# Kernel optimization log

Hardware: AMD Instinct MI355X
Metric: run time of the kernel (lower is better)

The kernel has to match this reference:

```python
import jax, jax.numpy as jnp
import numpy as np

NUM_FREQS = 10
N_POINTS = 500000
NUM_CLUSTERS = 64
KNN = 4
INPUT_CH = 3 + 3 * 2 * NUM_FREQS  # 63


def embed(x):
    # NeRF-style positional encoding: [x, sin(2^f x), cos(2^f x)] -> [N, 63]
    freqs = 2.0 ** jnp.arange(NUM_FREQS, dtype=x.dtype)          # [F]
    xf = x[:, None, :] * freqs[:, None]                           # [N, F, 3]
    n = x.shape[0]
    return jnp.concatenate(
        [x, jnp.sin(xf).reshape(n, -1), jnp.cos(xf).reshape(n, -1)], axis=-1)


def setup_inputs() -> dict:
    key = jax.random.key(0)
    ks = jax.random.split(key, 8)
    X = jax.random.normal(ks[0], (N_POINTS, 3), dtype=jnp.float32)
    cluster_ids = jax.random.randint(ks[1], (N_POINTS, KNN), 0, NUM_CLUSTERS)
    dist = jax.random.uniform(ks[2], (KNN, N_POINTS), dtype=jnp.float32)
    W_lin = jax.random.normal(ks[3], (NUM_CLUSTERS * 3, INPUT_CH), dtype=jnp.float32) * 0.05
    lambdas = jnp.ones((NUM_CLUSTERS,), dtype=jnp.float32) * 15.0
    # Only the first KNN MLPs can ever be dispatched (nearest = argmin over KNN rows)
    W0 = jax.random.normal(ks[4], (KNN, 256, 3 + INPUT_CH), dtype=jnp.float32) * 0.05
    W1 = jax.random.normal(ks[5], (KNN, 256, 256), dtype=jnp.float32) * 0.05
    W2 = jax.random.normal(ks[6], (KNN, 3, 256), dtype=jnp.float32) * 0.05
    return {"X": X, "cluster_ids": cluster_ids, "dist": dist, "W_lin": W_lin,
            "lambdas": lambdas, "W0": W0, "W1": W1, "W2": W2}


def _mlp(w0, w1, w2, x):
    h = jax.nn.relu(x @ w0.T)
    h = jax.nn.relu(h @ w1.T)
    return jnp.tanh(h @ w2.T)


def reference(X, cluster_ids, dist, W_lin, lambdas, W0, W1, W2):
    n = X.shape[0]
    # masked-out rays (-1,-1,-1) produce zeros; all math is per-point so we
    # compute densely and zero the masked rows at the end
    mask = (X[:, 0] == -1.0) & (X[:, 1] == -1.0) & (X[:, 2] == -1.0)  # [N]

    enc = embed(X)                                  # [N, 63]
    nearest = jnp.argmin(dist, axis=0)              # [N], values in [0, KNN)
    lam = lambdas[nearest]                          # [N]
    weights = jax.nn.softmax(lam * jnp.exp(-lam * dist), axis=0)  # [KNN, N]

    # per-cluster linear heads: [N, num_clusters, 3]
    lin = (enc @ W_lin.T).reshape(n, -1, 3)
    # knn gather + softmax-weighted combine -> [N, 3]
    gathered = jnp.take_along_axis(lin, cluster_ids[:, :, None], axis=1)  # [N, K, 3]
    combined = jnp.sum(gathered * weights.T[:, :, None], axis=1)          # [N, 3]

    inp = jnp.concatenate([combined, enc], axis=1)  # [N, 66]
    rgb = jnp.zeros((n, 3), dtype=X.dtype)
    for k in range(KNN):  # small fixed expert count
        out_k = _mlp(W0[k], W1[k], W2[k], inp)
        rgb = jnp.where((nearest == k)[:, None], out_k, rgb)

    return jnp.where(mask[:, None], 0.0, rgb)
```

## Files before the change

kernel.cpp:

```cpp
#include <hip/hip_runtime.h>
#include <cstdint>
#include <cstddef>

typedef _Float16 f16x8 __attribute__((ext_vector_type(8)));
typedef float    f32x4 __attribute__((ext_vector_type(4)));

#define TILE_M 128
#define WROWS  32

__global__ __launch_bounds__(256)
void k0_split(const float* __restrict__ W0, const float* __restrict__ W1,
              const float* __restrict__ W2, const float* __restrict__ Wlin,
              _Float16* __restrict__ W0h, _Float16* __restrict__ W0l,
              _Float16* __restrict__ W1h, _Float16* __restrict__ W1l,
              _Float16* __restrict__ W2h, _Float16* __restrict__ W2l,
              _Float16* __restrict__ WlinH, _Float16* __restrict__ WlinL)
{
    int idx = blockIdx.x * 256 + threadIdx.x;
    if (idx < 4*256*96) {
        int k = idx % 96; int en = idx / 96;
        float v = (k < 66) ? W0[en*66 + k] : 0.f;
        _Float16 h = (_Float16)v;
        W0h[idx] = h; W0l[idx] = (_Float16)(v - (float)h);
    }
    if (idx < 4*256*256) {
        float v = W1[idx];
        _Float16 h = (_Float16)v;
        W1h[idx] = h; W1l[idx] = (_Float16)(v - (float)h);
    }
    if (idx < 4*16*256) {
        int k = idx % 256; int er = idx / 256;
        int e = er / 16; int r = er % 16;
        float v = (r < 3) ? W2[(e*3 + r)*256 + k] : 0.f;
        _Float16 h = (_Float16)v;
        W2h[idx] = h; W2l[idx] = (_Float16)(v - (float)h);
    }
    if (idx < 192*64) {
        int k = idx & 63; int cc = idx >> 6;
        float v = (k < 63) ? Wlin[cc*63 + k] : 0.f;
        _Float16 h = (_Float16)v;
        WlinH[idx] = h; WlinL[idx] = (_Float16)(v - (float)h);
    }
}

#define MFMA16(A,B,C) __builtin_amdgcn_mfma_f32_16x16x32_f16(A, B, C, 0, 0, 0)

__global__ __launch_bounds__(256)
void k1_prep(const float* __restrict__ X, const int* __restrict__ cid,
             const float* __restrict__ dist,
             const _Float16* __restrict__ WlinH, const _Float16* __restrict__ WlinL,
             const float* __restrict__ lambdas,
             float* __restrict__ combined, int* __restrict__ order,
             int* __restrict__ cnt, int N)
{
    __shared__ _Float16 lins[4][32][200];
    __shared__ int hist[4];
    __shared__ int baseoff[4];
    int t = threadIdx.x;
    int wv = t >> 6, lane = t & 63, q = lane >> 4, lm = lane & 15;
    int blk = blockIdx.x;
    if (t < 4) hist[t] = 0;

    float xx[2][3];
    #pragma unroll
    for (int mt = 0; mt < 2; mt++) {
        int p = blk*128 + wv*32 + mt*16 + lm;
        bool v = (p < N);
        xx[mt][0] = v ? X[p*3+0] : 0.f;
        xx[mt][1] = v ? X[p*3+1] : 0.f;
        xx[mt][2] = v ? X[p*3+2] : 0.f;
    }
    f32x4 acc[2][12];
    #pragma unroll
    for (int mt = 0; mt < 2; mt++)
        #pragma unroll
        for (int nt = 0; nt < 12; nt++)
            acc[mt][nt] = (f32x4){0.f, 0.f, 0.f, 0.f};

    #pragma unroll
    for (int ks = 0; ks < 2; ks++) {
        f16x8 ah[2], al[2];
        #pragma unroll
        for (int mt = 0; mt < 2; mt++) {
            #pragma unroll
            for (int j = 0; j < 8; j++) {
                int c = ks*32 + q*8 + j;
                float v;
                if (c >= 63) v = 0.f;
                else if (c < 3) v = xx[mt][c];
                else {
                    int is_sin = (c < 33);
                    int s = is_sin ? (c - 3) : (c - 33);
                    int f = s / 3;
                    int d = s - f*3;
                    float arg = xx[mt][d] * (float)(1 << f);
                    float sv, cv;
                    sincosf(arg, &sv, &cv);
                    v = is_sin ? sv : cv;
                }
                _Float16 h = (_Float16)v;
                ah[mt][j] = h;
                al[mt][j] = (_Float16)(v - (float)h);
            }
        }
        #pragma unroll
        for (int nt = 0; nt < 12; nt++) {
            f16x8 bh = *(const f16x8*)(WlinH + (nt*16 + lm)*64 + ks*32 + q*8);
            f16x8 bl = *(const f16x8*)(WlinL + (nt*16 + lm)*64 + ks*32 + q*8);
            #pragma unroll
            for (int mt = 0; mt < 2; mt++) {
                acc[mt][nt] = MFMA16(ah[mt], bh, acc[mt][nt]);
                acc[mt][nt] = MFMA16(ah[mt], bl, acc[mt][nt]);
                acc[mt][nt] = MFMA16(al[mt], bh, acc[mt][nt]);
            }
        }
    }
    #pragma unroll
    for (int mt = 0; mt < 2; mt++)
        #pragma unroll
        for (int nt = 0; nt < 12; nt++)
            #pragma unroll
            for (int r = 0; r < 4; r++)
                lins[wv][mt*16 + q*4 + r][nt*16 + lm] = (_Float16)acc[mt][nt][r];
    __syncthreads();

    int near = 0, lrank = 0; bool valid = false; int p = 0;
    if (t < 128) {
        p = blk*128 + t;
        valid = (p < N);
        if (valid) {
            float d[4];
            #pragma unroll
            for (int k = 0; k < 4; k++) d[k] = dist[(size_t)k*N + p];
            float dmin = d[0]; near = 0;
            #pragma unroll
            for (int k = 1; k < 4; k++) if (d[k] < dmin) { dmin = d[k]; near = k; }
            float lam = lambdas[near];
            float s[4], wgt[4];
            #pragma unroll
            for (int k = 0; k < 4; k++) s[k] = lam * expf(-lam * d[k]);
            float m = fmaxf(fmaxf(s[0], s[1]), fmaxf(s[2], s[3]));
            float ssum = 0.f;
            #pragma unroll
            for (int k = 0; k < 4; k++) { wgt[k] = expf(s[k] - m); ssum += wgt[k]; }
            float inv = 1.f / ssum;
            int4 c4 = *(const int4*)(cid + p*4);
            int cks[4] = {c4.x, c4.y, c4.z, c4.w};
            int wv2 = t >> 5, r2 = t & 31;
            float c0 = 0.f, c1 = 0.f, c2 = 0.f;
            #pragma unroll
            for (int k = 0; k < 4; k++) {
                float wk = wgt[k] * inv;
                int b = cks[k] * 3;
                c0 += wk * (float)lins[wv2][r2][b+0];
                c1 += wk * (float)lins[wv2][r2][b+1];
                c2 += wk * (float)lins[wv2][r2][b+2];
            }
            combined[p*3+0] = c0; combined[p*3+1] = c1; combined[p*3+2] = c2;
            lrank = atomicAdd(&hist[near], 1);
        }
    }
    __syncthreads();
    if (t < 4) baseoff[t] = atomicAdd(&cnt[t], hist[t]);
    __syncthreads();
    if (valid) order[(size_t)near*N + baseoff[near] + lrank] = p;
}

__global__ __launch_bounds__(256, 1)
void k4_mlp(const float* __restrict__ X, const float* __restrict__ combined,
            const int* __restrict__ order, const int* __restrict__ cnt,
            const _Float16* __restrict__ W0h, const _Float16* __restrict__ W0l,
            const _Float16* __restrict__ W1h, const _Float16* __restrict__ W1l,
            const _Float16* __restrict__ W2h, const _Float16* __restrict__ W2l,
            float* __restrict__ out, int N, int tpe)
{
    __shared__ __align__(16) float hbuf[4][32][268];
    int e = blockIdx.x & 3;
    int tile = blockIdx.x >> 2;
    int count = cnt[e];
    int row0 = tile * TILE_M;
    if (row0 >= count) return;
    int wv   = threadIdx.x >> 6;
    int lane = threadIdx.x & 63;
    int q    = lane >> 4;
    int lm   = lane & 15;
    int wbase = row0 + wv * WROWS;
    const int* ord = order + (size_t)e * N + wbase;

    float xx[2][3], cb[2][3];
    #pragma unroll
    for (int mt = 0; mt < 2; mt++) {
        int r = mt*16 + lm;
        int pos = wbase + r;
        int p = (pos < count) ? ord[r] : 0;
        xx[mt][0] = X[p*3+0]; xx[mt][1] = X[p*3+1]; xx[mt][2] = X[p*3+2];
        cb[mt][0] = combined[p*3+0]; cb[mt][1] = combined[p*3+1]; cb[mt][2] = combined[p*3+2];
    }

    const _Float16* w0hb = W0h + e*(256*96);
    const _Float16* w0lb = W0l + e*(256*96);
    f32x4 acc[2][16];
    #pragma unroll
    for (int mt = 0; mt < 2; mt++)
        #pragma unroll
        for (int nt = 0; nt < 16; nt++)
            acc[mt][nt] = (f32x4){0.f, 0.f, 0.f, 0.f};

    #pragma unroll
    for (int ks = 0; ks < 3; ks++) {
        f16x8 ah[2], al[2];
        #pragma unroll
        for (int mt = 0; mt < 2; mt++) {
            #pragma unroll
            for (int j = 0; j < 8; j++) {
                int c = ks*32 + q*8 + j;
                float v;
                if (c >= 66) v = 0.f;
                else if (c < 3) v = (c==0) ? cb[mt][0] : ((c==1) ? cb[mt][1] : cb[mt][2]);
                else if (c < 6) v = (c==3) ? xx[mt][0] : ((c==4) ? xx[mt][1] : xx[mt][2]);
                else {
                    int is_sin = (c < 36);
                    int s = is_sin ? (c - 6) : (c - 36);
                    int f = s / 3;
                    int d = s - f*3;
                    float xd = (d==0) ? xx[mt][0] : ((d==1) ? xx[mt][1] : xx[mt][2]);
                    float arg = xd * (float)(1 << f);
                    float sv, cv;
                    sincosf(arg, &sv, &cv);
                    v = is_sin ? sv : cv;
                }
                _Float16 h = (_Float16)v;
                ah[mt][j] = h;
                al[mt][j] = (_Float16)(v - (float)h);
            }
        }
        #pragma unroll
        for (int nt = 0; nt < 16; nt++) {
            f16x8 bh = *(const f16x8*)(w0hb + (nt*16 + lm)*96 + ks*32 + q*8);
            f16x8 bl = *(const f16x8*)(w0lb + (nt*16 + lm)*96 + ks*32 + q*8);
            #pragma unroll
            for (int mt = 0; mt < 2; mt++) {
                acc[mt][nt] = MFMA16(ah[mt], bh, acc[mt][nt]);
                acc[mt][nt] = MFMA16(ah[mt], bl, acc[mt][nt]);
                acc[mt][nt] = MFMA16(al[mt], bh, acc[mt][nt]);
            }
        }
    }
    #pragma unroll
    for (int mt = 0; mt < 2; mt++)
        #pragma unroll
        for (int nt = 0; nt < 16; nt++)
            #pragma unroll
            for (int r = 0; r < 4; r++)
                hbuf[wv][mt*16 + q*4 + r][nt*16 + lm] = fmaxf(acc[mt][nt][r], 0.f);
    __syncthreads();

    const _Float16* w1hb = W1h + e*(256*256);
    const _Float16* w1lb = W1l + e*(256*256);
    #pragma unroll
    for (int mt = 0; mt < 2; mt++)
        #pragma unroll
        for (int nt = 0; nt < 16; nt++)
            acc[mt][nt] = (f32x4){0.f, 0.f, 0.f, 0.f};
    for (int ks = 0; ks < 8; ks++) {
        f16x8 ah[2], al[2];
        #pragma unroll
        for (int mt = 0; mt < 2; mt++) {
            const float* src = &hbuf[wv][mt*16 + lm][ks*32 + q*8];
            f32x4 va0 = *(const f32x4*)(src);
            f32x4 va1 = *(const f32x4*)(src + 4);
            #pragma unroll
            for (int j = 0; j < 8; j++) {
                float v = (j < 4) ? va0[j] : va1[j-4];
                _Float16 h = (_Float16)v;
                ah[mt][j] = h;
                al[mt][j] = (_Float16)(v - (float)h);
            }
        }
        #pragma unroll
        for (int nt = 0; nt < 16; nt++) {
            f16x8 bh = *(const f16x8*)(w1hb + (nt*16 + lm)*256 + ks*32 + q*8);
            f16x8 bl = *(const f16x8*)(w1lb + (nt*16 + lm)*256 + ks*32 + q*8);
            #pragma unroll
            for (int mt = 0; mt < 2; mt++) {
                acc[mt][nt] = MFMA16(ah[mt], bh, acc[mt][nt]);
                acc[mt][nt] = MFMA16(ah[mt], bl, acc[mt][nt]);
                acc[mt][nt] = MFMA16(al[mt], bh, acc[mt][nt]);
            }
        }
    }
    __syncthreads();
    #pragma unroll
    for (int mt = 0; mt < 2; mt++)
        #pragma unroll
        for (int nt = 0; nt < 16; nt++)
            #pragma unroll
            for (int r = 0; r < 4; r++)
                hbuf[wv][mt*16 + q*4 + r][nt*16 + lm] = fmaxf(acc[mt][nt][r], 0.f);
    __syncthreads();

    const _Float16* w2hb = W2h + e*(16*256);
    const _Float16* w2lb = W2l + e*(16*256);
    f32x4 acc3[2];
    acc3[0] = (f32x4){0.f,0.f,0.f,0.f};
    acc3[1] = (f32x4){0.f,0.f,0.f,0.f};
    for (int ks = 0; ks < 8; ks++) {
        f16x8 ah[2], al[2];
        #pragma unroll
        for (int mt = 0; mt < 2; mt++) {
            const float* src = &hbuf[wv][mt*16 + lm][ks*32 + q*8];
            f32x4 va0 = *(const f32x4*)(src);
            f32x4 va1 = *(const f32x4*)(src + 4);
            #pragma unroll
            for (int j = 0; j < 8; j++) {
                float v = (j < 4) ? va0[j] : va1[j-4];
                _Float16 h = (_Float16)v;
                ah[mt][j] = h;
                al[mt][j] = (_Float16)(v - (float)h);
            }
        }
        f16x8 bh = *(const f16x8*)(w2hb + lm*256 + ks*32 + q*8);
        f16x8 bl = *(const f16x8*)(w2lb + lm*256 + ks*32 + q*8);
        #pragma unroll
        for (int mt = 0; mt < 2; mt++) {
            acc3[mt] = MFMA16(ah[mt], bh, acc3[mt]);
            acc3[mt] = MFMA16(ah[mt], bl, acc3[mt]);
            acc3[mt] = MFMA16(al[mt], bh, acc3[mt]);
        }
    }
    if (lm < 3) {
        #pragma unroll
        for (int mt = 0; mt < 2; mt++)
            #pragma unroll
            for (int r = 0; r < 4; r++) {
                int row = mt*16 + q*4 + r;
                int pos = wbase + row;
                if (pos < count) {
                    int p = ord[row];
                    float x0 = X[p*3+0], x1 = X[p*3+1], x2 = X[p*3+2];
                    float msk = (x0 == -1.f && x1 == -1.f && x2 == -1.f) ? 0.f : 1.f;
                    out[p*3 + lm] = tanhf(acc3[mt][r]) * msk;
                }
            }
    }
}

extern "C" void kernel_launch(void* const* d_in, const int* in_sizes, int n_in,
                              void* d_out, int out_size, void* d_ws, size_t ws_size,
                              hipStream_t stream)
{
    const float* X    = (const float*)d_in[0];
    const int*   cid  = (const int*)  d_in[1];
    const float* dist = (const float*)d_in[2];
    const float* Wlin = (const float*)d_in[3];
    const float* lam  = (const float*)d_in[4];
    const float* W0   = (const float*)d_in[5];
    const float* W1   = (const float*)d_in[6];
    const float* W2   = (const float*)d_in[7];
    float* out = (float*)d_out;
    int N = in_sizes[0] / 3;

    char* ws = (char*)d_ws;
    size_t off = 0;
    int* cnt = (int*)(ws + off);           off += 256;
    float* combined = (float*)(ws + off);  off += (size_t)N * 3 * sizeof(float);
    off = (off + 255) & ~(size_t)255;
    int* order = (int*)(ws + off);         off += (size_t)4 * N * sizeof(int);
    off = (off + 255) & ~(size_t)255;
    _Float16* W0h = (_Float16*)(ws + off); off += (size_t)4*256*96*2;
    _Float16* W0l = (_Float16*)(ws + off); off += (size_t)4*256*96*2;
    _Float16* W1h = (_Float16*)(ws + off); off += (size_t)4*256*256*2;
    _Float16* W1l = (_Float16*)(ws + off); off += (size_t)4*256*256*2;
    _Float16* W2h = (_Float16*)(ws + off); off += (size_t)4*16*256*2;
    _Float16* W2l = (_Float16*)(ws + off); off += (size_t)4*16*256*2;
    _Float16* WlinH = (_Float16*)(ws + off); off += (size_t)192*64*2;
    _Float16* WlinL = (_Float16*)(ws + off); off += (size_t)192*64*2;

    hipMemsetAsync(cnt, 0, 4 * sizeof(int), stream);
    k0_split<<<dim3((4*256*256 + 255)/256), dim3(256), 0, stream>>>(
        W0, W1, W2, Wlin, W0h, W0l, W1h, W1l, W2h, W2l, WlinH, WlinL);
    k1_prep<<<dim3((N + 127)/128), dim3(256), 0, stream>>>(
        X, cid, dist, WlinH, WlinL, lam, combined, order, cnt, N);
    int tpe = (N + TILE_M - 1) / TILE_M;
    k4_mlp<<<dim3(4*tpe), dim3(256), 0, stream>>>(
        X, combined, order, cnt, W0h, W0l, W1h, W1l, W2h, W2l, out, N, tpe);
}
```

Before: 1.117 ms.

## Halve MLP tile rows per wave for two blocks per CU with setprio

Each wave of the expert-MLP kernel now handles 16 rows instead of 32, so the tile drops to 64 rows and the shared buffer shrinks to half. With the accumulator registers halved, launch bounds allow two blocks per CU, and the block-wide syncthreads are removed because each wave only touches its own shared slice. s_setprio is raised around the MFMA loops so waves that are issuing matrix work get scheduling priority. The cost is that each weight fragment loaded from memory now feeds half as many MFMAs, so weight traffic per point doubles.

```diff
diff --git a/kernel.cpp b/kernel.cpp
--- a/kernel.cpp
+++ b/kernel.cpp
@@ -5,8 +5,7 @@
 typedef _Float16 f16x8 __attribute__((ext_vector_type(8)));
 typedef float    f32x4 __attribute__((ext_vector_type(4)));
 
-#define TILE_M 128
-#define WROWS  32
+#define TILE_M 64
 
 __global__ __launch_bounds__(256)
 void k0_split(const float* __restrict__ W0, const float* __restrict__ W1,
@@ -166,7 +165,7 @@
     if (valid) order[(size_t)near*N + baseoff[near] + lrank] = p;
 }
 
-__global__ __launch_bounds__(256, 1)
+__global__ __launch_bounds__(256, 2)
 void k4_mlp(const float* __restrict__ X, const float* __restrict__ combined,
             const int* __restrict__ order, const int* __restrict__ cnt,
             const _Float16* __restrict__ W0h, const _Float16* __restrict__ W0l,
@@ -174,7 +173,7 @@
             const _Float16* __restrict__ W2h, const _Float16* __restrict__ W2l,
             float* __restrict__ out, int N, int tpe)
 {
-    __shared__ __align__(16) float hbuf[4][32][268];
+    __shared__ __align__(16) float hbuf[4][16][268];
     int e = blockIdx.x & 3;
     int tile = blockIdx.x >> 2;
     int count = cnt[e];
@@ -184,164 +183,137 @@
     int lane = threadIdx.x & 63;
     int q    = lane >> 4;
     int lm   = lane & 15;
-    int wbase = row0 + wv * WROWS;
+    int wbase = row0 + wv * 16;
     const int* ord = order + (size_t)e * N + wbase;
 
-    float xx[2][3], cb[2][3];
-    #pragma unroll
-    for (int mt = 0; mt < 2; mt++) {
-        int r = mt*16 + lm;
-        int pos = wbase + r;
-        int p = (pos < count) ? ord[r] : 0;
-        xx[mt][0] = X[p*3+0]; xx[mt][1] = X[p*3+1]; xx[mt][2] = X[p*3+2];
-        cb[mt][0] = combined[p*3+0]; cb[mt][1] = combined[p*3+1]; cb[mt][2] = combined[p*3+2];
+    float xx[3], cb[3];
+    {
+        int pos = wbase + lm;
+        int p = (pos < count) ? ord[lm] : 0;
+        xx[0] = X[p*3+0]; xx[1] = X[p*3+1]; xx[2] = X[p*3+2];
+        cb[0] = combined[p*3+0]; cb[1] = combined[p*3+1]; cb[2] = combined[p*3+2];
     }
 
     const _Float16* w0hb = W0h + e*(256*96);
     const _Float16* w0lb = W0l + e*(256*96);
-    f32x4 acc[2][16];
-    #pragma unroll
-    for (int mt = 0; mt < 2; mt++)
-        #pragma unroll
-        for (int nt = 0; nt < 16; nt++)
-            acc[mt][nt] = (f32x4){0.f, 0.f, 0.f, 0.f};
+    f32x4 acc[16];
+    #pragma unroll
+    for (int nt = 0; nt < 16; nt++)
+        acc[nt] = (f32x4){0.f, 0.f, 0.f, 0.f};
 
     #pragma unroll
     for (int ks = 0; ks < 3; ks++) {
-        f16x8 ah[2], al[2];
-        #pragma unroll
-        for (int mt = 0; mt < 2; mt++) {
-            #pragma unroll
-            for (int j = 0; j < 8; j++) {
-                int c = ks*32 + q*8 + j;
-                float v;
-                if (c >= 66) v = 0.f;
-                else if (c < 3) v = (c==0) ? cb[mt][0] : ((c==1) ? cb[mt][1] : cb[mt][2]);
-                else if (c < 6) v = (c==3) ? xx[mt][0] : ((c==4) ? xx[mt][1] : xx[mt][2]);
-                else {
-                    int is_sin = (c < 36);
-                    int s = is_sin ? (c - 6) : (c - 36);
-                    int f = s / 3;
-                    int d = s - f*3;
-                    float xd = (d==0) ? xx[mt][0] : ((d==1) ? xx[mt][1] : xx[mt][2]);
-                    float arg = xd * (float)(1 << f);
-                    float sv, cv;
-                    sincosf(arg, &sv, &cv);
-                    v = is_sin ? sv : cv;
-                }
-                _Float16 h = (_Float16)v;
-                ah[mt][j] = h;
-                al[mt][j] = (_Float16)(v - (float)h);
-            }
-        }
+        f16x8 ah, al;
+        #pragma unroll
+        for (int j = 0; j < 8; j++) {
+            int c = ks*32 + q*8 + j;
+            float v;
+            if (c >= 66) v = 0.f;
+            else if (c < 3) v = (c==0) ? cb[0] : ((c==1) ? cb[1] : cb[2]);
+            else if (c < 6) v = (c==3) ? xx[0] : ((c==4) ? xx[1] : xx[2]);
+            else {
+                int is_sin = (c < 36);
+                int s = is_sin ? (c - 6) : (c - 36);
+                int f = s / 3;
+                int d = s - f*3;
+                float xd = (d==0) ? xx[0] : ((d==1) ? xx[1] : xx[2]);
+                float arg = xd * (float)(1 << f);
+                float sv, cv;
+                sincosf(arg, &sv, &cv);
+                v = is_sin ? sv : cv;
+            }
+            _Float16 h = (_Float16)v;
+            ah[j] = h;
+            al[j] = (_Float16)(v - (float)h);
+        }
+        __builtin_amdgcn_s_setprio(1);
         #pragma unroll
         for (int nt = 0; nt < 16; nt++) {
             f16x8 bh = *(const f16x8*)(w0hb + (nt*16 + lm)*96 + ks*32 + q*8);
             f16x8 bl = *(const f16x8*)(w0lb + (nt*16 + lm)*96 + ks*32 + q*8);
-            #pragma unroll
-            for (int mt = 0; mt < 2; mt++) {
-                acc[mt][nt] = MFMA16(ah[mt], bh, acc[mt][nt]);
-                acc[mt][nt] = MFMA16(ah[mt], bl, acc[mt][nt]);
-                acc[mt][nt] = MFMA16(al[mt], bh, acc[mt][nt]);
-            }
-        }
-    }
-    #pragma unroll
-    for (int mt = 0; mt < 2; mt++)
-        #pragma unroll
-        for (int nt = 0; nt < 16; nt++)
-            #pragma unroll
-            for (int r = 0; r < 4; r++)
-                hbuf[wv][mt*16 + q*4 + r][nt*16 + lm] = fmaxf(acc[mt][nt][r], 0.f);
-    __syncthreads();
+            acc[nt] = MFMA16(ah, bh, acc[nt]);
+            acc[nt] = MFMA16(ah, bl, acc[nt]);
+            acc[nt] = MFMA16(al, bh, acc[nt]);
+        }
+        __builtin_amdgcn_s_setprio(0);
+    }
+    #pragma unroll
+    for (int nt = 0; nt < 16; nt++)
+        #pragma unroll
+        for (int r = 0; r < 4; r++)
+            hbuf[wv][q*4 + r][nt*16 + lm] = fmaxf(acc[nt][r], 0.f);
 
     const _Float16* w1hb = W1h + e*(256*256);
     const _Float16* w1lb = W1l + e*(256*256);
     #pragma unroll
-    for (int mt = 0; mt < 2; mt++)
-        #pragma unroll
-        for (int nt = 0; nt < 16; nt++)
-            acc[mt][nt] = (f32x4){0.f, 0.f, 0.f, 0.f};
+    for (int nt = 0; nt < 16; nt++)
+        acc[nt] = (f32x4){0.f, 0.f, 0.f, 0.f};
     for (int ks = 0; ks < 8; ks++) {
-        f16x8 ah[2], al[2];
-        #pragma unroll
-        for (int mt = 0; mt < 2; mt++) {
-            const float* src = &hbuf[wv][mt*16 + lm][ks*32 + q*8];
+        f16x8 ah, al;
+        {
+            const float* src = &hbuf[wv][lm][ks*32 + q*8];
             f32x4 va0 = *(const f32x4*)(src);
             f32x4 va1 = *(const f32x4*)(src + 4);
             #pragma unroll
             for (int j = 0; j < 8; j++) {
                 float v = (j < 4) ? va0[j] : va1[j-4];
                 _Float16 h = (_Float16)v;
-                ah[mt][j] = h;
-                al[mt][j] = (_Float16)(v - (float)h);
-            }
-        }
+                ah[j] = h;
+                al[j] = (_Float16)(v - (float)h);
+            }
+        }
+        __builtin_amdgcn_s_setprio(1);
         #pragma unroll
         for (int nt = 0; nt < 16; nt++) {
             f16x8 bh = *(const f16x8*)(w1hb + (nt*16 + lm)*256 + ks*32 + q*8);
             f16x8 bl = *(const f16x8*)(w1lb + (nt*16 + lm)*256 + ks*32 + q*8);
-            #pragma unroll
-            for (int mt = 0; mt < 2; mt++) {
-                acc[mt][nt] = MFMA16(ah[mt], bh, acc[mt][nt]);
-                acc[mt][nt] = MFMA16(ah[mt], bl, acc[mt][nt]);
-                acc[mt][nt] = MFMA16(al[mt], bh, acc[mt][nt]);
-            }
-        }
-    }
-    __syncthreads();
-    #pragma unroll
-    for (int mt = 0; mt < 2; mt++)
-        #pragma unroll
-        for (int nt = 0; nt < 16; nt++)
-            #pragma unroll
-            for (int r = 0; r < 4; r++)
-                hbuf[wv][mt*16 + q*4 + r][nt*16 + lm] = fmaxf(acc[mt][nt][r], 0.f);
-    __syncthreads();
+            acc[nt] = MFMA16(ah, bh, acc[nt]);
+            acc[nt] = MFMA16(ah, bl, acc[nt]);
+            acc[nt] = MFMA16(al, bh, acc[nt]);
+        }
+        __builtin_amdgcn_s_setprio(0);
+    }
+    #pragma unroll
+    for (int nt = 0; nt < 16; nt++)
+        #pragma unroll
+        for (int r = 0; r < 4; r++)
+            hbuf[wv][q*4 + r][nt*16 + lm] = fmaxf(acc[nt][r], 0.f);
 
     const _Float16* w2hb = W2h + e*(16*256);
     const _Float16* w2lb = W2l + e*(16*256);
-    f32x4 acc3[2];
-    acc3[0] = (f32x4){0.f,0.f,0.f,0.f};
-    acc3[1] = (f32x4){0.f,0.f,0.f,0.f};
+    f32x4 acc3 = (f32x4){0.f,0.f,0.f,0.f};
     for (int ks = 0; ks < 8; ks++) {
-        f16x8 ah[2], al[2];
-        #pragma unroll
-        for (int mt = 0; mt < 2; mt++) {
-            const float* src = &hbuf[wv][mt*16 + lm][ks*32 + q*8];
+        f16x8 ah, al;
+        {
+            const float* src = &hbuf[wv][lm][ks*32 + q*8];
             f32x4 va0 = *(const f32x4*)(src);
             f32x4 va1 = *(const f32x4*)(src + 4);
             #pragma unroll
             for (int j = 0; j < 8; j++) {
                 float v = (j < 4) ? va0[j] : va1[j-4];
                 _Float16 h = (_Float16)v;
-                ah[mt][j] = h;
-                al[mt][j] = (_Float16)(v - (float)h);
+                ah[j] = h;
+                al[j] = (_Float16)(v - (float)h);
             }
         }
         f16x8 bh = *(const f16x8*)(w2hb + lm*256 + ks*32 + q*8);
         f16x8 bl = *(const f16x8*)(w2lb + lm*256 + ks*32 + q*8);
-        #pragma unroll
-        for (int mt = 0; mt < 2; mt++) {
-            acc3[mt] = MFMA16(ah[mt], bh, acc3[mt]);
-            acc3[mt] = MFMA16(ah[mt], bl, acc3[mt]);
-            acc3[mt] = MFMA16(al[mt], bh, acc3[mt]);
-        }
+        acc3 = MFMA16(ah, bh, acc3);
+        acc3 = MFMA16(ah, bl, acc3);
+        acc3 = MFMA16(al, bh, acc3);
     }
     if (lm < 3) {
         #pragma unroll
-        for (int mt = 0; mt < 2; mt++)
-            #pragma unroll
-            for (int r = 0; r < 4; r++) {
-                int row = mt*16 + q*4 + r;
-                int pos = wbase + row;
-                if (pos < count) {
-                    int p = ord[row];
-                    float x0 = X[p*3+0], x1 = X[p*3+1], x2 = X[p*3+2];
-                    float msk = (x0 == -1.f && x1 == -1.f && x2 == -1.f) ? 0.f : 1.f;
-                    out[p*3 + lm] = tanhf(acc3[mt][r]) * msk;
-                }
-            }
+        for (int r = 0; r < 4; r++) {
+            int row = q*4 + r;
+            int pos = wbase + row;
+            if (pos < count) {
+                int p = ord[row];
+                float x0 = X[p*3+0], x1 = X[p*3+1], x2 = X[p*3+2];
+                float msk = (x0 == -1.f && x1 == -1.f && x2 == -1.f) ? 0.f : 1.f;
+                out[p*3 + lm] = tanhf(acc3[r]) * msk;
+            }
+        }
     }
 }
 
```

Result: slower. 1.423 ms (+27.3%).
